# Performance work log

Hardware: AMD Instinct MI355X
Metric: run time of the kernel (lower is better)

The kernel has to match this reference:

```python
import jax, jax.numpy as jnp
import numpy as np

N_EMBD = 1024
NUM_HEADS = 16
HEAD_DIM = N_EMBD // NUM_HEADS
B, N = 4, 1024
EPS = 1e-5


def _ln(x, w, b):
    mu = jnp.mean(x, axis=-1, keepdims=True)
    var = jnp.var(x, axis=-1, keepdims=True)
    return (x - mu) * jax.lax.rsqrt(var + EPS) * w + b


def setup_inputs() -> dict:
    key = jax.random.key(0)
    ks = jax.random.split(key, 12)
    s = 0.02
    d, dff = N_EMBD, 4 * N_EMBD
    return {
        "x": jax.random.normal(ks[0], (B, N, d), dtype=jnp.float32),
        "ln1_w": jnp.ones((d,), jnp.float32),
        "ln1_b": jnp.zeros((d,), jnp.float32),
        "Wq": jax.random.normal(ks[1], (d, d), jnp.float32) * s,
        "bq": jnp.zeros((d,), jnp.float32),
        "Wk": jax.random.normal(ks[2], (d, d), jnp.float32) * s,
        "bk": jnp.zeros((d,), jnp.float32),
        "Wv": jax.random.normal(ks[3], (d, d), jnp.float32) * s,
        "bv": jnp.zeros((d,), jnp.float32),
        "Wo": jax.random.normal(ks[4], (d, d), jnp.float32) * s,
        "bo": jnp.zeros((d,), jnp.float32),
        "ln2_w": jnp.ones((d,), jnp.float32),
        "ln2_b": jnp.zeros((d,), jnp.float32),
        "Wfc": jax.random.normal(ks[5], (d, dff), jnp.float32) * s,
        "bfc": jnp.zeros((dff,), jnp.float32),
        "Wproj": jax.random.normal(ks[6], (dff, d), jnp.float32) * s,
        "bproj": jnp.zeros((d,), jnp.float32),
    }


def reference(x, ln1_w, ln1_b, Wq, bq, Wk, bk, Wv, bv, Wo, bo,
              ln2_w, ln2_b, Wfc, bfc, Wproj, bproj):
    # --- attention sublayer ---
    h = _ln(x, ln1_w, ln1_b)  # [B,N,D]
    q = (h @ Wq + bq).reshape(B, N, NUM_HEADS, HEAD_DIM).transpose(0, 2, 1, 3)
    k = (h @ Wk + bk).reshape(B, N, NUM_HEADS, HEAD_DIM).transpose(0, 2, 1, 3)
    v = (h @ Wv + bv).reshape(B, N, NUM_HEADS, HEAD_DIM).transpose(0, 2, 1, 3)
    scale = 1.0 / np.sqrt(HEAD_DIM).astype(np.float32)
    attn = jax.nn.softmax(jnp.einsum("bhqd,bhkd->bhqk", q, k) * scale, axis=-1)
    o = jnp.einsum("bhqk,bhkd->bhqd", attn, v)  # [B,H,N,Dh]
    o = o.transpose(0, 2, 1, 3).reshape(B, N, N_EMBD)
    x = x + (o @ Wo + bo)
    # --- MLP sublayer (exact GELU, matching torch nn.GELU default) ---
    h2 = _ln(x, ln2_w, ln2_b)
    h2 = jax.nn.gelu(h2 @ Wfc + bfc, approximate=False)
    x = x + (h2 @ Wproj + bproj)
    return x
```

## Files before the change

### kernel.cpp

```cpp
#include <hip/hip_runtime.h>
#include <hip/hip_bf16.h>

typedef unsigned short u16;
typedef u16 u16x8 __attribute__((ext_vector_type(8)));
typedef u16 u16x4 __attribute__((ext_vector_type(4)));
typedef __bf16 bf16x8 __attribute__((ext_vector_type(8)));
typedef float f32x4 __attribute__((ext_vector_type(4)));

__device__ __forceinline__ u16 f2bf(float f) {
  union { __hip_bfloat16 h; u16 u; } cv;
  cv.h = __float2bfloat16(f);
  return cv.u;
}
__device__ __forceinline__ float bf2f(u16 u) {
  union { unsigned u; float f; } c;
  c.u = ((unsigned)u) << 16;
  return c.f;
}

__device__ __forceinline__ void glds16(const void* g, void* l) {
  __builtin_amdgcn_global_load_lds(
      (const __attribute__((address_space(1))) unsigned int*)g,
      (__attribute__((address_space(3))) unsigned int*)l, 16, 0, 0);
}

__global__ __launch_bounds__(256) void transpose_bf16(const float* __restrict__ W,
                                                      u16* __restrict__ Wt,
                                                      int K, int N) {
  __shared__ float tile[32][33];
  int tx = threadIdx.x, ty = threadIdx.y;
  int n0 = blockIdx.x * 32, k0 = blockIdx.y * 32;
#pragma unroll
  for (int j = 0; j < 4; ++j)
    tile[ty + j * 8][tx] = W[(size_t)(k0 + ty + j * 8) * N + n0 + tx];
  __syncthreads();
#pragma unroll
  for (int j = 0; j < 4; ++j)
    Wt[(size_t)(n0 + ty + j * 8) * K + k0 + tx] = f2bf(tile[tx][ty + j * 8]);
}

__global__ __launch_bounds__(256) void transpose4(const float* __restrict__ W0,
                                                  const float* __restrict__ W1,
                                                  const float* __restrict__ W2,
                                                  const float* __restrict__ W3,
                                                  u16* __restrict__ T0, u16* __restrict__ T1,
                                                  u16* __restrict__ T2, u16* __restrict__ T3) {
  __shared__ float tile[32][33];
  int z = blockIdx.z;
  const float* W = (z == 0) ? W0 : (z == 1) ? W1 : (z == 2) ? W2 : W3;
  u16* T = (z == 0) ? T0 : (z == 1) ? T1 : (z == 2) ? T2 : T3;
  int tx = threadIdx.x, ty = threadIdx.y;
  int n0 = blockIdx.x * 32, k0 = blockIdx.y * 32;
#pragma unroll
  for (int j = 0; j < 4; ++j)
    tile[ty + j * 8][tx] = W[(size_t)(k0 + ty + j * 8) * 1024 + n0 + tx];
  __syncthreads();
#pragma unroll
  for (int j = 0; j < 4; ++j)
    T[(size_t)(n0 + ty + j * 8) * 1024 + k0 + tx] = f2bf(tile[tx][ty + j * 8]);
}

__global__ __launch_bounds__(256) void ln_kernel(const float* __restrict__ x,
                                                 const float* __restrict__ w,
                                                 const float* __restrict__ b,
                                                 u16* __restrict__ out) {
  int row = blockIdx.x, t = threadIdx.x;
  const float* xr = x + (size_t)row * 1024;
  float4 v = *reinterpret_cast<const float4*>(xr + t * 4);
  float s = v.x + v.y + v.z + v.w;
  float s2 = v.x * v.x + v.y * v.y + v.z * v.z + v.w * v.w;
#pragma unroll
  for (int m = 1; m < 64; m <<= 1) {
    s += __shfl_xor(s, m, 64);
    s2 += __shfl_xor(s2, m, 64);
  }
  __shared__ float red[8];
  if ((t & 63) == 0) { red[t >> 6] = s; red[(t >> 6) + 4] = s2; }
  __syncthreads();
  s = red[0] + red[1] + red[2] + red[3];
  s2 = red[4] + red[5] + red[6] + red[7];
  float mu = s * (1.f / 1024.f);
  float var = s2 * (1.f / 1024.f) - mu * mu;
  float rs = rsqrtf(var + 1e-5f);
  float4 wv = *reinterpret_cast<const float4*>(w + t * 4);
  float4 bv = *reinterpret_cast<const float4*>(b + t * 4);
  u16x4 o;
  o.x = f2bf((v.x - mu) * rs * wv.x + bv.x);
  o.y = f2bf((v.y - mu) * rs * wv.y + bv.y);
  o.z = f2bf((v.z - mu) * rs * wv.z + bv.z);
  o.w = f2bf((v.w - mu) * rs * wv.w + bv.w);
  *reinterpret_cast<u16x4*>(out + (size_t)row * 1024 + t * 4) = o;
}

template <int MODE>
__global__ __launch_bounds__(512, 2) void gemm256(
    const u16* __restrict__ A, const u16* __restrict__ Bt,
    const float* __restrict__ b0, const float* __restrict__ b1,
    const float* __restrict__ b2,
    u16* __restrict__ o0, u16* __restrict__ o1, u16* __restrict__ o2,
    u16* __restrict__ o3,
    int Kfull, int KL, int MT, int NT, float qscale) {
  __shared__ u16 lds[2][2][2][256 * 32];
  const int tid = threadIdx.x;
  const int lane = tid & 63, w = tid >> 6;
  const int wm = w >> 2, wn = w & 3;
  const int l15 = lane & 15, l4 = lane >> 4;
  const int skey = (l15 >> 1) & 3;

  const int nwg = gridDim.x;
  int wg = (int)blockIdx.x;
  wg = (wg & 7) * (nwg >> 3) + (wg >> 3);
  const int mt = wg % MT;
  int rest = wg / MT;
  const int nt = rest % NT;
  const int zt = rest / NT;

  const int row0 = mt * 256, col0 = nt * 256;
  const int kbase = zt * KL;
  const int nkt = KL >> 6;

  auto stageAB = [&](int buf, int ks, int kt) {
    const int kb = kbase + (kt << 6) + (ks << 5);
#pragma unroll
    for (int i = 0; i < 2; ++i) {
      int c = i * 512 + tid;
      int r = c >> 2, sch = (c & 3) ^ ((r >> 1) & 3);
      glds16(A + (size_t)(row0 + r) * Kfull + kb + sch * 8, &lds[buf][0][ks][0] + c * 8);
    }
#pragma unroll
    for (int i = 0; i < 2; ++i) {
      int c = i * 512 + tid;
      int r = c >> 2, sch = (c & 3) ^ ((r >> 1) & 3);
      glds16(Bt + (size_t)(col0 + r) * Kfull + kb + sch * 8, &lds[buf][1][ks][0] + c * 8);
    }
  };
  auto rdA = [&](int buf, int ks, int m) -> bf16x8 {
    int row = wm * 128 + m * 16 + l15;
    return *reinterpret_cast<const bf16x8*>(&lds[buf][0][ks][row * 32 + ((l4 ^ skey) << 3)]);
  };
  auto rdB = [&](int buf, int ks, int n) -> bf16x8 {
    int row = wn * 64 + n * 16 + l15;
    return *reinterpret_cast<const bf16x8*>(&lds[buf][1][ks][row * 32 + ((l4 ^ skey) << 3)]);
  };

  f32x4 acc[8][4];
#pragma unroll
  for (int m = 0; m < 8; ++m)
#pragma unroll
    for (int n = 0; n < 4; ++n) acc[m][n] = (f32x4){0.f, 0.f, 0.f, 0.f};

  stageAB(0, 0, 0);
  stageAB(0, 1, 0);
  asm volatile("s_waitcnt vmcnt(4)" ::: "memory");
  __builtin_amdgcn_s_barrier();

  bf16x8 am[4], bn[4];
  for (int t = 0; t < nkt; ++t) {
    const int cur = t & 1, nxt = cur ^ 1;
    const bool pf = (t + 1 < nkt);
    {
#pragma unroll
      for (int m = 0; m < 4; ++m) am[m] = rdA(cur, 0, m);
#pragma unroll
      for (int n = 0; n < 4; ++n) bn[n] = rdB(cur, 0, n);
      if (pf) stageAB(nxt, 0, t + 1);
      __builtin_amdgcn_s_barrier();
      __builtin_amdgcn_s_setprio(1);
#pragma unroll
      for (int m = 0; m < 4; ++m)
#pragma unroll
        for (int n = 0; n < 4; ++n)
          acc[m][n] = __builtin_amdgcn_mfma_f32_16x16x32_bf16(am[m], bn[n], acc[m][n], 0, 0, 0);
      __builtin_amdgcn_s_setprio(0);
    }
    {
#pragma unroll
      for (int m = 0; m < 4; ++m) am[m] = rdA(cur, 0, m + 4);
      if (pf) {
        asm volatile("s_waitcnt vmcnt(4)" ::: "memory");
      } else {
        asm volatile("s_waitcnt vmcnt(0)" ::: "memory");
      }
      __builtin_amdgcn_s_barrier();
      __builtin_amdgcn_s_setprio(1);
#pragma unroll
      for (int m = 0; m < 4; ++m)
#pragma unroll
        for (int n = 0; n < 4; ++n)
          acc[m + 4][n] = __builtin_amdgcn_mfma_f32_16x16x32_bf16(am[m], bn[n], acc[m + 4][n], 0, 0, 0);
      __builtin_amdgcn_s_setprio(0);
    }
    {
#pragma unroll
      for (int m = 0; m < 4; ++m) am[m] = rdA(cur, 1, m);
#pragma unroll
      for (int n = 0; n < 4; ++n) bn[n] = rdB(cur, 1, n);
      if (pf) stageAB(nxt, 1, t + 1);
      __builtin_amdgcn_s_barrier();
      __builtin_amdgcn_s_setprio(1);
#pragma unroll
      for (int m = 0; m < 4; ++m)
#pragma unroll
        for (int n = 0; n < 4; ++n)
          acc[m][n] = __builtin_amdgcn_mfma_f32_16x16x32_bf16(am[m], bn[n], acc[m][n], 0, 0, 0);
      __builtin_amdgcn_s_setprio(0);
    }
    {
#pragma unroll
      for (int m = 0; m < 4; ++m) am[m] = rdA(cur, 1, m + 4);
      asm volatile("s_waitcnt vmcnt(4)" ::: "memory");
      __builtin_amdgcn_s_barrier();
      __builtin_amdgcn_s_setprio(1);
#pragma unroll
      for (int m = 0; m < 4; ++m)
#pragma unroll
        for (int n = 0; n < 4; ++n)
          acc[m + 4][n] = __builtin_amdgcn_mfma_f32_16x16x32_bf16(am[m], bn[n], acc[m + 4][n], 0, 0, 0);
      __builtin_amdgcn_s_setprio(0);
    }
  }

  if constexpr (MODE == 0) {
    const int which = nt >> 2;
    const int bidx = mt >> 2;
#pragma unroll
    for (int m = 0; m < 8; ++m)
#pragma unroll
      for (int n = 0; n < 4; ++n) {
        int colc = (col0 & 1023) + wn * 64 + n * 16 + l15;
        int hh = colc >> 6, d = colc & 63;
        int nb = (row0 & 1023) + wm * 128 + m * 16 + l4 * 4;
        if (which == 2) {
          u16x4 pk;
#pragma unroll
          for (int r = 0; r < 4; ++r) pk[r] = f2bf(acc[m][n][r] + b2[colc]);
          *reinterpret_cast<u16x4*>(o2 + (((size_t)(bidx * 16 + hh) * 64 + d) * 1024 + nb)) = pk;
        } else {
          const float* bb = (which == 0) ? b0 : b1;
          u16* dst = (which == 0) ? o0 : o1;
          float sc = (which == 0) ? qscale : 1.0f;
#pragma unroll
          for (int r = 0; r < 4; ++r)
            dst[((size_t)(bidx * 16 + hh) * 1024 + nb + r) * 64 + d] =
                f2bf((acc[m][n][r] + bb[colc]) * sc);
        }
      }
  } else if constexpr (MODE == 2) {
    const int N = NT * 256;
#pragma unroll
    for (int m = 0; m < 8; ++m)
#pragma unroll
      for (int n = 0; n < 4; ++n)
#pragma unroll
        for (int r = 0; r < 4; ++r) {
          int row = row0 + wm * 128 + m * 16 + l4 * 4 + r;
          int col = col0 + wn * 64 + n * 16 + l15;
          float val = acc[m][n][r] + b0[col];
          float g = 0.5f * val * (1.0f + erff(val * 0.70710678118f));
          o0[(size_t)row * N + col] = f2bf(g);
        }
  } else {
    const int N = NT * 256;
    u16* base = (zt == 0) ? o0 : (zt == 1) ? o1 : (zt == 2) ? o2 : o3;
#pragma unroll
    for (int m = 0; m < 8; ++m)
#pragma unroll
      for (int n = 0; n < 4; ++n)
#pragma unroll
        for (int r = 0; r < 4; ++r) {
          int row = row0 + wm * 128 + m * 16 + l4 * 4 + r;
          int col = col0 + wn * 64 + n * 16 + l15;
          base[(size_t)row * N + col] = f2bf(acc[m][n][r]);
        }
  }
}

__global__ __launch_bounds__(256) void reduce4(const u16* __restrict__ p0,
                                               const u16* __restrict__ p1,
                                               const u16* __restrict__ p2,
                                               const u16* __restrict__ p3,
                                               const float* __restrict__ bias,
                                               const float* __restrict__ res,
                                               float* __restrict__ out) {
  size_t i = ((size_t)blockIdx.x * 256 + threadIdx.x) * 8;
  int col = (int)(i & 1023);
  float s[8];
  float4 r0 = *reinterpret_cast<const float4*>(res + i);
  float4 r1 = *reinterpret_cast<const float4*>(res + i + 4);
  s[0] = r0.x; s[1] = r0.y; s[2] = r0.z; s[3] = r0.w;
  s[4] = r1.x; s[5] = r1.y; s[6] = r1.z; s[7] = r1.w;
#pragma unroll
  for (int j = 0; j < 8; ++j) s[j] += bias[col + j];
  const u16* ps[4] = {p0, p1, p2, p3};
#pragma unroll
  for (int sp = 0; sp < 4; ++sp) {
    u16x8 pv = *reinterpret_cast<const u16x8*>(ps[sp] + i);
#pragma unroll
    for (int j = 0; j < 8; ++j) s[j] += bf2f(pv[j]);
  }
  float4 o0 = {s[0], s[1], s[2], s[3]};
  float4 o1 = {s[4], s[5], s[6], s[7]};
  *reinterpret_cast<float4*>(out + i) = o0;
  *reinterpret_cast<float4*>(out + i + 4) = o1;
}

__global__ __launch_bounds__(256) void reduce_ln(const u16* __restrict__ p0,
                                                 const u16* __restrict__ p1,
                                                 const u16* __restrict__ p2,
                                                 const u16* __restrict__ p3,
                                                 const float* __restrict__ bias,
                                                 const float* __restrict__ res,
                                                 const float* __restrict__ lnw,
                                                 const float* __restrict__ lnb,
                                                 float* __restrict__ x1,
                                                 u16* __restrict__ h2out) {
  int row = blockIdx.x, t = threadIdx.x;
  size_t i = (size_t)row * 1024 + t * 4;
  int col = t * 4;
  float4 r = *reinterpret_cast<const float4*>(res + i);
  float4 bi = *reinterpret_cast<const float4*>(bias + col);
  float v0 = r.x + bi.x, v1 = r.y + bi.y, v2 = r.z + bi.z, v3 = r.w + bi.w;
  const u16* ps[4] = {p0, p1, p2, p3};
#pragma unroll
  for (int sp = 0; sp < 4; ++sp) {
    u16x4 pv = *reinterpret_cast<const u16x4*>(ps[sp] + i);
    v0 += bf2f(pv[0]); v1 += bf2f(pv[1]); v2 += bf2f(pv[2]); v3 += bf2f(pv[3]);
  }
  float4 xo = {v0, v1, v2, v3};
  *reinterpret_cast<float4*>(x1 + i) = xo;

  float s = v0 + v1 + v2 + v3;
  float s2 = v0 * v0 + v1 * v1 + v2 * v2 + v3 * v3;
#pragma unroll
  for (int m = 1; m < 64; m <<= 1) {
    s += __shfl_xor(s, m, 64);
    s2 += __shfl_xor(s2, m, 64);
  }
  __shared__ float red[8];
  if ((t & 63) == 0) { red[t >> 6] = s; red[(t >> 6) + 4] = s2; }
  __syncthreads();
  s = red[0] + red[1] + red[2] + red[3];
  s2 = red[4] + red[5] + red[6] + red[7];
  float mu = s * (1.f / 1024.f);
  float var = s2 * (1.f / 1024.f) - mu * mu;
  float rs = rsqrtf(var + 1e-5f);
  float4 wv = *reinterpret_cast<const float4*>(lnw + col);
  float4 bv = *reinterpret_cast<const float4*>(lnb + col);
  u16x4 o;
  o.x = f2bf((v0 - mu) * rs * wv.x + bv.x);
  o.y = f2bf((v1 - mu) * rs * wv.y + bv.y);
  o.z = f2bf((v2 - mu) * rs * wv.z + bv.z);
  o.w = f2bf((v3 - mu) * rs * wv.w + bv.w);
  *reinterpret_cast<u16x4*>(h2out + i) = o;
}

__global__ __launch_bounds__(256) void attn_kernel(const u16* __restrict__ q,
                                                   const u16* __restrict__ k,
                                                   const u16* __restrict__ vt,
                                                   u16* __restrict__ o) {
  const int bh = blockIdx.x, qb = blockIdx.y;
  const int b = bh >> 4, h = bh & 15;
  __shared__ u16 Ks[2][4096];
  __shared__ u16 Vt[2][4096];
  __shared__ u16 Ps[4][1024];
  const int tid = threadIdx.x, lane = tid & 63, w = tid >> 6;
  const int l15 = lane & 15, l4 = lane >> 4;
  const int sw = l15 & 7;
  const u16* kbase = k + (size_t)bh * 65536;
  const u16* vtbase = vt + (size_t)bh * 65536;

  const u16* qrow = q + ((size_t)bh * 1024 + qb * 64 + w * 16 + l15) * 64;
  bf16x8 qf0 = *reinterpret_cast<const bf16x8*>(qrow + l4 * 8);
  bf16x8 qf1 = *reinterpret_cast<const bf16x8*>(qrow + 32 + l4 * 8);

  auto stageKV = [&](int buf, int kv0) {
#pragma unroll
    for (int i = 0; i < 2; ++i) {
      int c = i * 256 + tid, r = c >> 3, sl = (c & 7) ^ (r & 7);
      glds16(kbase + (size_t)(kv0 + r) * 64 + sl * 8, &Ks[buf][c * 8]);
    }
#pragma unroll
    for (int i = 0; i < 2; ++i) {
      int c = i * 256 + tid, r = c >> 3, sl = (c & 7) ^ (r & 7);
      glds16(vtbase + (size_t)r * 1024 + kv0 + sl * 8, &Vt[buf][c * 8]);
    }
  };

  f32x4 oacc[4];
#pragma unroll
  for (int n = 0; n < 4; ++n) oacc[n] = (f32x4){0.f, 0.f, 0.f, 0.f};
  float mrow = -3.0e38f, lrow = 0.f;

  stageKV(0, 0);
  __syncthreads();

  for (int kv0 = 0; kv0 < 1024; kv0 += 64) {
    int cur = (kv0 >> 6) & 1;
    if (kv0 + 64 < 1024) stageKV(cur ^ 1, kv0 + 64);

    f32x4 st[4];
#pragma unroll
    for (int t = 0; t < 4; ++t) {
      int row = t * 16 + l15;
      f32x4 s = (f32x4){0.f, 0.f, 0.f, 0.f};
      bf16x8 kf0 = *reinterpret_cast<const bf16x8*>(&Ks[cur][row * 64 + ((l4 ^ sw) << 3)]);
      s = __builtin_amdgcn_mfma_f32_16x16x32_bf16(kf0, qf0, s, 0, 0, 0);
      bf16x8 kf1 = *reinterpret_cast<const bf16x8*>(&Ks[cur][row * 64 + (((4 + l4) ^ sw) << 3)]);
      s = __builtin_amdgcn_mfma_f32_16x16x32_bf16(kf1, qf1, s, 0, 0, 0);
      st[t] = s;
    }

    float tm = st[0][0];
#pragma unroll
    for (int t = 0; t < 4; ++t)
#pragma unroll
      for (int r = 0; r < 4; ++r) tm = fmaxf(tm, st[t][r]);
    tm = fmaxf(tm, __shfl_xor(tm, 16, 64));
    tm = fmaxf(tm, __shfl_xor(tm, 32, 64));
    if (!__all(tm - mrow <= 8.f)) {
      float mnew = fmaxf(mrow, tm);
      float al = exp2f(mrow - mnew);
      lrow *= al;
#pragma unroll
      for (int n = 0; n < 4; ++n)
#pragma unroll
        for (int r = 0; r < 4; ++r) oacc[n][r] *= al;
      mrow = mnew;
    }
    float pr[4][4];
    float ps = 0.f;
#pragma unroll
    for (int t = 0; t < 4; ++t)
#pragma unroll
      for (int r = 0; r < 4; ++r) {
        pr[t][r] = exp2f(st[t][r] - mrow);
        ps += pr[t][r];
      }
    ps += __shfl_xor(ps, 16, 64);
    ps += __shfl_xor(ps, 32, 64);
    lrow += ps;

#pragma unroll
    for (int t = 0; t < 4; ++t) {
      u16x4 pk;
#pragma unroll
      for (int r = 0; r < 4; ++r) pk[r] = f2bf(pr[t][r]);
      int swch = ((t << 1) | (l4 >> 1)) ^ sw;
      *reinterpret_cast<u16x4*>(&Ps[w][l15 * 64 + swch * 8 + (l4 & 1) * 4]) = pk;
    }

#pragma unroll
    for (int c2 = 0; c2 < 2; ++c2) {
      bf16x8 pf = *reinterpret_cast<const bf16x8*>(
          &Ps[w][l15 * 64 + ((((c2 << 2) | l4) ^ sw) << 3)]);
#pragma unroll
      for (int n = 0; n < 4; ++n) {
        bf16x8 vf = *reinterpret_cast<const bf16x8*>(
            &Vt[cur][(n * 16 + l15) * 64 + ((((c2 << 2) | l4) ^ sw) << 3)]);
        oacc[n] = __builtin_amdgcn_mfma_f32_16x16x32_bf16(vf, pf, oacc[n], 0, 0, 0);
      }
    }
    __syncthreads();
  }

  float inv = 1.0f / lrow;
  int nr = qb * 64 + w * 16 + l15;
#pragma unroll
  for (int n = 0; n < 4; ++n) {
    u16x4 pk;
#pragma unroll
    for (int r = 0; r < 4; ++r) pk[r] = f2bf(oacc[n][r] * inv);
    *reinterpret_cast<u16x4*>(
        o + ((size_t)(b * 1024 + nr)) * 1024 + h * 64 + n * 16 + l4 * 4) = pk;
  }
}

extern "C" void kernel_launch(void* const* d_in, const int* in_sizes, int n_in,
                              void* d_out, int out_size, void* d_ws, size_t ws_size,
                              hipStream_t stream) {
  (void)in_sizes; (void)n_in; (void)out_size; (void)ws_size;
  const float* x     = (const float*)d_in[0];
  const float* ln1w  = (const float*)d_in[1];
  const float* ln1b  = (const float*)d_in[2];
  const float* Wq    = (const float*)d_in[3];
  const float* bq    = (const float*)d_in[4];
  const float* Wk    = (const float*)d_in[5];
  const float* bk    = (const float*)d_in[6];
  const float* Wv    = (const float*)d_in[7];
  const float* bv    = (const float*)d_in[8];
  const float* Wo    = (const float*)d_in[9];
  const float* bo    = (const float*)d_in[10];
  const float* ln2w  = (const float*)d_in[11];
  const float* ln2b  = (const float*)d_in[12];
  const float* Wfc   = (const float*)d_in[13];
  const float* bfc   = (const float*)d_in[14];
  const float* Wproj = (const float*)d_in[15];
  const float* bproj = (const float*)d_in[16];
  float* out = (float*)d_out;

  char* p = (char*)d_ws;
  u16* hb     = (u16*)p; p += (size_t)4096 * 1024 * 2;
  u16* WqkvT  = (u16*)p; p += (size_t)3072 * 1024 * 2;
  u16* WoT    = (u16*)p; p += (size_t)1024 * 1024 * 2;
  u16* WfcT   = (u16*)p; p += (size_t)4096 * 1024 * 2;
  u16* WprojT = (u16*)p; p += (size_t)1024 * 4096 * 2;
  u16* qb_    = (u16*)p; p += (size_t)4096 * 1024 * 2;
  u16* kb_    = (u16*)p; p += (size_t)4096 * 1024 * 2;
  u16* vt_    = (u16*)p; p += (size_t)4096 * 1024 * 2;
  u16* ob_    = (u16*)p; p += (size_t)4096 * 1024 * 2;
  float* x1   = (float*)p; p += (size_t)4096 * 1024 * 4;
  u16* h2     = (u16*)p; p += (size_t)4096 * 1024 * 2;
  u16* ffnb   = (u16*)p; p += (size_t)4096 * 4096 * 2;

  const float qscale = 0.125f * 1.44269504089f;

  dim3 tb(32, 8);
  transpose4<<<dim3(32, 32, 4), tb, 0, stream>>>(Wq, Wk, Wv, Wo,
                                                 WqkvT, WqkvT + (size_t)1024 * 1024,
                                                 WqkvT + (size_t)2048 * 1024, WoT);
  transpose_bf16<<<dim3(128, 32), tb, 0, stream>>>(Wfc, WfcT, 1024, 4096);
  transpose_bf16<<<dim3(32, 128), tb, 0, stream>>>(Wproj, WprojT, 4096, 1024);

  ln_kernel<<<4096, 256, 0, stream>>>(x, ln1w, ln1b, hb);

  gemm256<0><<<192, 512, 0, stream>>>(hb, WqkvT, bq, bk, bv,
                                      qb_, kb_, vt_, nullptr, 1024, 1024, 16, 12, qscale);

  attn_kernel<<<dim3(64, 16), 256, 0, stream>>>(qb_, kb_, vt_, ob_);

  gemm256<3><<<256, 512, 0, stream>>>(ob_, WoT, nullptr, nullptr, nullptr,
                                      qb_, kb_, vt_, h2, 1024, 256, 16, 4, 1.f);
  reduce_ln<<<4096, 256, 0, stream>>>(qb_, kb_, vt_, h2, bo, x, ln2w, ln2b, x1, hb);

  gemm256<2><<<256, 512, 0, stream>>>(hb, WfcT, bfc, nullptr, nullptr,
                                      ffnb, nullptr, nullptr, nullptr, 1024, 1024, 16, 16, 1.f);

  gemm256<3><<<256, 512, 0, stream>>>(ffnb, WprojT, nullptr, nullptr, nullptr,
                                      qb_, kb_, vt_, ob_, 4096, 1024, 16, 4, 1.f);
  reduce4<<<2048, 256, 0, stream>>>(qb_, kb_, vt_, ob_, bproj, x1, out);
}
```

Before: 339.6 us.

## Shrink GEMM tiles to 128x128 with simpler double-buffered K loop

Replaces the 256x256 GEMM tile (512 threads, 64-wide K step split into two halves, fine-grained waitcnt/barrier phasing) with a 128x128 tile of 256 threads and a single 32-wide K step per iteration, using plain __syncthreads double buffering. Grid sizes grow 4x (e.g. 768/1024 blocks) to fill more CUs and raise occupancy. The cost is lower arithmetic intensity per tile, more global/LDS traffic per FLOP, and the loss of the hand-tuned interleaving of loads and MFMAs.

```diff
diff --git a/kernel.cpp b/kernel.cpp
--- a/kernel.cpp
+++ b/kernel.cpp
@@ -93,17 +93,17 @@
 }
 
 template <int MODE>
-__global__ __launch_bounds__(512, 2) void gemm256(
+__global__ __launch_bounds__(256, 3) void gemm128(
     const u16* __restrict__ A, const u16* __restrict__ Bt,
     const float* __restrict__ b0, const float* __restrict__ b1,
     const float* __restrict__ b2,
     u16* __restrict__ o0, u16* __restrict__ o1, u16* __restrict__ o2,
     u16* __restrict__ o3,
     int Kfull, int KL, int MT, int NT, float qscale) {
-  __shared__ u16 lds[2][2][2][256 * 32];
+  __shared__ u16 lds[2][2][128 * 32];
   const int tid = threadIdx.x;
   const int lane = tid & 63, w = tid >> 6;
-  const int wm = w >> 2, wn = w & 3;
+  const int wm = w >> 1, wn = w & 1;
   const int l15 = lane & 15, l4 = lane >> 4;
   const int skey = (l15 >> 1) & 3;
 
@@ -115,121 +115,71 @@
   const int nt = rest % NT;
   const int zt = rest / NT;
 
-  const int row0 = mt * 256, col0 = nt * 256;
+  const int row0 = mt * 128, col0 = nt * 128;
   const int kbase = zt * KL;
-  const int nkt = KL >> 6;
-
-  auto stageAB = [&](int buf, int ks, int kt) {
-    const int kb = kbase + (kt << 6) + (ks << 5);
+  const int nkt = KL >> 5;
+
+  auto stageAB = [&](int buf, int kt) {
+    const int kb = kbase + (kt << 5);
 #pragma unroll
     for (int i = 0; i < 2; ++i) {
-      int c = i * 512 + tid;
+      int c = i * 256 + tid;
       int r = c >> 2, sch = (c & 3) ^ ((r >> 1) & 3);
-      glds16(A + (size_t)(row0 + r) * Kfull + kb + sch * 8, &lds[buf][0][ks][0] + c * 8);
+      glds16(A + (size_t)(row0 + r) * Kfull + kb + sch * 8, &lds[buf][0][0] + c * 8);
     }
 #pragma unroll
     for (int i = 0; i < 2; ++i) {
-      int c = i * 512 + tid;
+      int c = i * 256 + tid;
       int r = c >> 2, sch = (c & 3) ^ ((r >> 1) & 3);
-      glds16(Bt + (size_t)(col0 + r) * Kfull + kb + sch * 8, &lds[buf][1][ks][0] + c * 8);
+      glds16(Bt + (size_t)(col0 + r) * Kfull + kb + sch * 8, &lds[buf][1][0] + c * 8);
     }
   };
-  auto rdA = [&](int buf, int ks, int m) -> bf16x8 {
-    int row = wm * 128 + m * 16 + l15;
-    return *reinterpret_cast<const bf16x8*>(&lds[buf][0][ks][row * 32 + ((l4 ^ skey) << 3)]);
+  auto rdA = [&](int buf, int m) -> bf16x8 {
+    int row = wm * 64 + m * 16 + l15;
+    return *reinterpret_cast<const bf16x8*>(&lds[buf][0][row * 32 + ((l4 ^ skey) << 3)]);
   };
-  auto rdB = [&](int buf, int ks, int n) -> bf16x8 {
+  auto rdB = [&](int buf, int n) -> bf16x8 {
     int row = wn * 64 + n * 16 + l15;
-    return *reinterpret_cast<const bf16x8*>(&lds[buf][1][ks][row * 32 + ((l4 ^ skey) << 3)]);
+    return *reinterpret_cast<const bf16x8*>(&lds[buf][1][row * 32 + ((l4 ^ skey) << 3)]);
   };
 
-  f32x4 acc[8][4];
-#pragma unroll
-  for (int m = 0; m < 8; ++m)
+  f32x4 acc[4][4];
+#pragma unroll
+  for (int m = 0; m < 4; ++m)
 #pragma unroll
     for (int n = 0; n < 4; ++n) acc[m][n] = (f32x4){0.f, 0.f, 0.f, 0.f};
 
-  stageAB(0, 0, 0);
-  stageAB(0, 1, 0);
-  asm volatile("s_waitcnt vmcnt(4)" ::: "memory");
-  __builtin_amdgcn_s_barrier();
-
-  bf16x8 am[4], bn[4];
+  stageAB(0, 0);
+  __syncthreads();
+
   for (int t = 0; t < nkt; ++t) {
-    const int cur = t & 1, nxt = cur ^ 1;
-    const bool pf = (t + 1 < nkt);
-    {
-#pragma unroll
-      for (int m = 0; m < 4; ++m) am[m] = rdA(cur, 0, m);
-#pragma unroll
-      for (int n = 0; n < 4; ++n) bn[n] = rdB(cur, 0, n);
-      if (pf) stageAB(nxt, 0, t + 1);
-      __builtin_amdgcn_s_barrier();
-      __builtin_amdgcn_s_setprio(1);
-#pragma unroll
-      for (int m = 0; m < 4; ++m)
-#pragma unroll
-        for (int n = 0; n < 4; ++n)
-          acc[m][n] = __builtin_amdgcn_mfma_f32_16x16x32_bf16(am[m], bn[n], acc[m][n], 0, 0, 0);
-      __builtin_amdgcn_s_setprio(0);
-    }
-    {
-#pragma unroll
-      for (int m = 0; m < 4; ++m) am[m] = rdA(cur, 0, m + 4);
-      if (pf) {
-        asm volatile("s_waitcnt vmcnt(4)" ::: "memory");
-      } else {
-        asm volatile("s_waitcnt vmcnt(0)" ::: "memory");
-      }
-      __builtin_amdgcn_s_barrier();
-      __builtin_amdgcn_s_setprio(1);
-#pragma unroll
-      for (int m = 0; m < 4; ++m)
-#pragma unroll
-        for (int n = 0; n < 4; ++n)
-          acc[m + 4][n] = __builtin_amdgcn_mfma_f32_16x16x32_bf16(am[m], bn[n], acc[m + 4][n], 0, 0, 0);
-      __builtin_amdgcn_s_setprio(0);
-    }
-    {
-#pragma unroll
-      for (int m = 0; m < 4; ++m) am[m] = rdA(cur, 1, m);
-#pragma unroll
-      for (int n = 0; n < 4; ++n) bn[n] = rdB(cur, 1, n);
-      if (pf) stageAB(nxt, 1, t + 1);
-      __builtin_amdgcn_s_barrier();
-      __builtin_amdgcn_s_setprio(1);
-#pragma unroll
-      for (int m = 0; m < 4; ++m)
-#pragma unroll
-        for (int n = 0; n < 4; ++n)
-          acc[m][n] = __builtin_amdgcn_mfma_f32_16x16x32_bf16(am[m], bn[n], acc[m][n], 0, 0, 0);
-      __builtin_amdgcn_s_setprio(0);
-    }
-    {
-#pragma unroll
-      for (int m = 0; m < 4; ++m) am[m] = rdA(cur, 1, m + 4);
-      asm volatile("s_waitcnt vmcnt(4)" ::: "memory");
-      __builtin_amdgcn_s_barrier();
-      __builtin_amdgcn_s_setprio(1);
-#pragma unroll
-      for (int m = 0; m < 4; ++m)
-#pragma unroll
-        for (int n = 0; n < 4; ++n)
-          acc[m + 4][n] = __builtin_amdgcn_mfma_f32_16x16x32_bf16(am[m], bn[n], acc[m + 4][n], 0, 0, 0);
-      __builtin_amdgcn_s_setprio(0);
-    }
+    const int cur = t & 1;
+    if (t + 1 < nkt) stageAB(cur ^ 1, t + 1);
+    bf16x8 af[4], bfr[4];
+#pragma unroll
+    for (int m = 0; m < 4; ++m) af[m] = rdA(cur, m);
+#pragma unroll
+    for (int n = 0; n < 4; ++n) bfr[n] = rdB(cur, n);
+    __builtin_amdgcn_s_setprio(1);
+#pragma unroll
+    for (int m = 0; m < 4; ++m)
+#pragma unroll
+      for (int n = 0; n < 4; ++n)
+        acc[m][n] = __builtin_amdgcn_mfma_f32_16x16x32_bf16(af[m], bfr[n], acc[m][n], 0, 0, 0);
+    __builtin_amdgcn_s_setprio(0);
+    __syncthreads();
   }
 
   if constexpr (MODE == 0) {
-    const int which = nt >> 2;
-    const int bidx = mt >> 2;
-#pragma unroll
-    for (int m = 0; m < 8; ++m)
+    const int which = nt >> 3;
+    const int bidx = mt >> 3;
+#pragma unroll
+    for (int m = 0; m < 4; ++m)
 #pragma unroll
       for (int n = 0; n < 4; ++n) {
-        int colc = (col0 & 1023) + wn * 64 + n * 16 + l15;
+        int colc = (nt & 7) * 128 + wn * 64 + n * 16 + l15;
         int hh = colc >> 6, d = colc & 63;
-        int nb = (row0 & 1023) + wm * 128 + m * 16 + l4 * 4;
+        int nb = (mt & 7) * 128 + wm * 64 + m * 16 + l4 * 4;
         if (which == 2) {
           u16x4 pk;
 #pragma unroll
@@ -246,29 +196,29 @@
         }
       }
   } else if constexpr (MODE == 2) {
-    const int N = NT * 256;
-#pragma unroll
-    for (int m = 0; m < 8; ++m)
+    const int N = NT * 128;
+#pragma unroll
+    for (int m = 0; m < 4; ++m)
 #pragma unroll
       for (int n = 0; n < 4; ++n)
 #pragma unroll
         for (int r = 0; r < 4; ++r) {
-          int row = row0 + wm * 128 + m * 16 + l4 * 4 + r;
+          int row = row0 + wm * 64 + m * 16 + l4 * 4 + r;
           int col = col0 + wn * 64 + n * 16 + l15;
           float val = acc[m][n][r] + b0[col];
           float g = 0.5f * val * (1.0f + erff(val * 0.70710678118f));
           o0[(size_t)row * N + col] = f2bf(g);
         }
   } else {
-    const int N = NT * 256;
+    const int N = NT * 128;
     u16* base = (zt == 0) ? o0 : (zt == 1) ? o1 : (zt == 2) ? o2 : o3;
 #pragma unroll
-    for (int m = 0; m < 8; ++m)
+    for (int m = 0; m < 4; ++m)
 #pragma unroll
       for (int n = 0; n < 4; ++n)
 #pragma unroll
         for (int r = 0; r < 4; ++r) {
-          int row = row0 + wm * 128 + m * 16 + l4 * 4 + r;
+          int row = row0 + wm * 64 + m * 16 + l4 * 4 + r;
           int col = col0 + wn * 64 + n * 16 + l15;
           base[(size_t)row * N + col] = f2bf(acc[m][n][r]);
         }
@@ -523,19 +473,19 @@
 
   ln_kernel<<<4096, 256, 0, stream>>>(x, ln1w, ln1b, hb);
 
-  gemm256<0><<<192, 512, 0, stream>>>(hb, WqkvT, bq, bk, bv,
-                                      qb_, kb_, vt_, nullptr, 1024, 1024, 16, 12, qscale);
+  gemm128<0><<<768, 256, 0, stream>>>(hb, WqkvT, bq, bk, bv,
+                                      qb_, kb_, vt_, nullptr, 1024, 1024, 32, 24, qscale);
 
   attn_kernel<<<dim3(64, 16), 256, 0, stream>>>(qb_, kb_, vt_, ob_);
 
-  gemm256<3><<<256, 512, 0, stream>>>(ob_, WoT, nullptr, nullptr, nullptr,
-                                      qb_, kb_, vt_, h2, 1024, 256, 16, 4, 1.f);
+  gemm128<3><<<1024, 256, 0, stream>>>(ob_, WoT, nullptr, nullptr, nullptr,
+                                       qb_, kb_, vt_, h2, 1024, 256, 32, 8, 1.f);
   reduce_ln<<<4096, 256, 0, stream>>>(qb_, kb_, vt_, h2, bo, x, ln2w, ln2b, x1, hb);
 
-  gemm256<2><<<256, 512, 0, stream>>>(hb, WfcT, bfc, nullptr, nullptr,
-                                      ffnb, nullptr, nullptr, nullptr, 1024, 1024, 16, 16, 1.f);
-
-  gemm256<3><<<256, 512, 0, stream>>>(ffnb, WprojT, nullptr, nullptr, nullptr,
-                                      qb_, kb_, vt_, ob_, 4096, 1024, 16, 4, 1.f);
+  gemm128<2><<<1024, 256, 0, stream>>>(hb, WfcT, bfc, nullptr, nullptr,
+                                       ffnb, nullptr, nullptr, nullptr, 1024, 1024, 32, 32, 1.f);
+
+  gemm128<3><<<1024, 256, 0, stream>>>(ffnb, WprojT, nullptr, nullptr, nullptr,
+                                       qb_, kb_, vt_, ob_, 4096, 1024, 32, 8, 1.f);
   reduce4<<<2048, 256, 0, stream>>>(qb_, kb_, vt_, ob_, bproj, x1, out);
 }
```

After: 355.4 us. +4.6%, slower.
